# Kernel tuning notes

Hardware: AMD Instinct MI355X
Metric: run time of the kernel (lower is better)

Reference implementation:

```python
import jax, jax.numpy as jnp
import numpy as np

N_NODES, N_EDGES, D_IN, D_OUT = 50000, 800000, 64, 64
N_REL, N_TIME = 500, 1000


def setup_inputs() -> dict:
    key = jax.random.key(0)
    ks = jax.random.split(key, 14)
    xavier = lambda k, shape: jax.random.normal(k, shape, jnp.float32) * np.sqrt(2.0 / (shape[0] + shape[1])) * np.sqrt(2.0)
    return {
        "x": jax.random.normal(ks[0], (N_NODES, D_IN), jnp.float32),
        "rel_repr": jax.random.normal(ks[1], (N_REL, D_IN), jnp.float32),
        "time_emds": jax.random.normal(ks[2], (N_TIME, D_IN), jnp.float32),
        "src": jax.random.randint(ks[3], (N_EDGES,), 0, N_NODES),
        "dst": jax.random.randint(ks[4], (N_EDGES,), 0, N_NODES),
        "etype": jax.random.randint(ks[5], (N_EDGES,), 0, N_REL),
        "etime": jax.random.randint(ks[6], (N_EDGES,), 0, N_TIME),
        "trans_w": xavier(ks[7], (D_IN, D_OUT)),
        "loop_w": xavier(ks[8], (D_IN, D_OUT)),
        "w_rel": xavier(ks[9], (D_IN, D_OUT)),
        "attn_h": xavier(ks[10], (D_IN, 1)),
        "attn_t": xavier(ks[11], (D_IN, 1)),
        "attn_r": xavier(ks[12], (D_IN, 1)),
        "attn_ts": xavier(ks[13], (D_IN, 1)),
    }


def reference(x, rel_repr, time_emds, src, dst, etype, etime,
              trans_w, loop_w, w_rel, attn_h, attn_t, attn_r, attn_ts):
    n = x.shape[0]
    # per-node / per-rel / per-time scalar attention projections
    h_att = (x @ attn_h)[:, 0]          # [N]
    t_att = (x @ attn_t)[:, 0]          # [N]
    r_att = (rel_repr @ attn_r)[:, 0]   # [R]
    ts_att = (time_emds @ attn_ts)[:, 0]  # [T]
    # edge attention logits + edge_softmax grouped by destination node
    e = jax.nn.leaky_relu(h_att[src] - t_att[dst] + r_att[etype] + ts_att[etime], 0.1)  # [E]
    m = jax.ops.segment_max(e, dst, num_segments=n)
    ex = jnp.exp(e - m[dst])
    den = jax.ops.segment_sum(ex, dst, num_segments=n)
    att = (ex / den[dst])[:, None]      # [E,1]
    # message: (head + time) * (rel + time) -> trans_w -> weighted scatter-sum to dst
    time_emd = time_emds[etime]         # [E,D]
    edge_data = (x[src] + time_emd) * (rel_repr[etype] + time_emd)
    msg = (edge_data @ trans_w) * att   # [E,D_out]
    h = jax.ops.segment_sum(msg, dst, num_segments=n)
    x_out = h + x @ loop_w
    rel_out = rel_repr @ w_rel
    return (x_out, rel_out)
```

## Files before the change

### kernel.cpp

```cpp
#include <hip/hip_runtime.h>
#include <hip/hip_bf16.h>

#define N_NODES 50000
#define N_EDGES 800000
#define D 64
#define N_REL 500
#define N_TIME 1000
#define SLOTS 64
#define NODE_BLOCKS ((N_NODES + 63) / 64)
#define REL_BLOCKS  ((N_REL + 63) / 64)

__device__ __forceinline__ float bf2f(unsigned short u) {
    union { unsigned int i; float f; } v;
    v.i = ((unsigned int)u) << 16;
    return v.f;
}

__global__ void proj_kernel(const float* __restrict__ x,
                            const float* __restrict__ rel,
                            const float* __restrict__ tim,
                            const float* __restrict__ ah,
                            const float* __restrict__ at,
                            const float* __restrict__ ar,
                            const float* __restrict__ ats,
                            float* __restrict__ h_att, float* __restrict__ t_att,
                            float* __restrict__ r_att, float* __restrict__ ts_att,
                            unsigned short* __restrict__ x_bf) {
    int wave = (blockIdx.x * blockDim.x + threadIdx.x) >> 6;
    int lane = threadIdx.x & 63;
    const int total = N_NODES + N_REL + N_TIME;
    if (wave >= total) return;
    if (wave < N_NODES) {
        float xv = x[wave * D + lane];
        __hip_bfloat16 b = __float2bfloat16(xv);
        x_bf[wave * D + lane] = *(unsigned short*)&b;
        float s1 = xv * ah[lane];
        float s2 = xv * at[lane];
        for (int off = 32; off; off >>= 1) {
            s1 += __shfl_down(s1, off);
            s2 += __shfl_down(s2, off);
        }
        if (lane == 0) { h_att[wave] = s1; t_att[wave] = s2; }
    } else if (wave < N_NODES + N_REL) {
        int r = wave - N_NODES;
        float v = rel[r * D + lane] * ar[lane];
        for (int off = 32; off; off >>= 1) v += __shfl_down(v, off);
        if (lane == 0) r_att[r] = v;
    } else {
        int t = wave - N_NODES - N_REL;
        float v = tim[t * D + lane] * ats[lane];
        for (int off = 32; off; off >>= 1) v += __shfl_down(v, off);
        if (lane == 0) ts_att[t] = v;
    }
}

__global__ void build_kernel(const int* __restrict__ src, const int* __restrict__ dst,
                             const int* __restrict__ etype, const int* __restrict__ etime,
                             const float* __restrict__ h_att, const float* __restrict__ t_att,
                             const float* __restrict__ r_att, const float* __restrict__ ts_att,
                             int* __restrict__ cnt, int2* __restrict__ payload) {
    int e = blockIdx.x * blockDim.x + threadIdx.x;
    if (e >= N_EDGES) return;
    int s = src[e], d = dst[e], r = etype[e], t = etime[e];
    float lg = h_att[s] - t_att[d] + r_att[r] + ts_att[t];
    float lr = lg > 0.f ? lg : 0.1f * lg;
    float ex = __expf(lr);
    unsigned exb = __float_as_uint(ex);
    int2 pl;
    pl.x = (int)((exb & ~7u) | (unsigned)(s & 7));
    pl.y = (int)(((unsigned)(s >> 3) << 19) | ((unsigned)r << 10) | (unsigned)t);
    int pos = atomicAdd(&cnt[d], 1);
    if (pos < SLOTS) payload[(d << 6) + pos] = pl;
}

__global__ void node_gather_kernel(const unsigned short* __restrict__ x_bf,
                                   const float* __restrict__ rel,
                                   const float* __restrict__ tim,
                                   const int* __restrict__ cnt,
                                   const int2* __restrict__ payload,
                                   float* __restrict__ agg) {
    int d = (blockIdx.x * blockDim.x + threadIdx.x) >> 6;
    int lane = threadIdx.x & 63;
    if (d >= N_NODES) return;
    int deg = cnt[d];
    if (deg > SLOTS) deg = SLOTS;

    int s_l = 0, r_l = 0, t_l = 0;
    float ex = 0.f;
    if (lane < deg) {
        int2 pl = payload[(d << 6) + lane];
        unsigned px = (unsigned)pl.x;
        unsigned py = (unsigned)pl.y;
        ex = __uint_as_float(px & ~7u);
        s_l = (int)(((py >> 19) << 3) | (px & 7u));
        r_l = (int)((py >> 10) & 511u);
        t_l = (int)(py & 1023u);
    }
    float den = ex;
    for (int off = 32; off; off >>= 1) den += __shfl_xor(den, off);
    float att_l = (lane < deg) ? ex / den : 0.f;

    int qw = lane >> 4;
    int ql = lane & 15;
    float4 acc = make_float4(0.f, 0.f, 0.f, 0.f);
    for (int i = 0; i < deg; i += 4) {
        int ei = i + qw;
        int s = __shfl(s_l, ei);
        int r = __shfl(r_l, ei);
        int t = __shfl(t_l, ei);
        float att = __shfl(att_l, ei);
        float4  te = *(const float4*)(tim + t * D + ql * 4);
        ushort4 xb = *(const ushort4*)(x_bf + s * D + ql * 4);
        float4  rl = *(const float4*)(rel + r * D + ql * 4);
        acc.x += att * (bf2f(xb.x) + te.x) * (rl.x + te.x);
        acc.y += att * (bf2f(xb.y) + te.y) * (rl.y + te.y);
        acc.z += att * (bf2f(xb.z) + te.z) * (rl.z + te.z);
        acc.w += att * (bf2f(xb.w) + te.w) * (rl.w + te.w);
    }
    for (int off = 16; off <= 32; off <<= 1) {
        acc.x += __shfl_xor(acc.x, off);
        acc.y += __shfl_xor(acc.y, off);
        acc.z += __shfl_xor(acc.z, off);
        acc.w += __shfl_xor(acc.w, off);
    }
    if (qw == 0)
        *(float4*)(agg + (d << 7) + ql * 4) = acc;
}

__global__ __launch_bounds__(256, 4)
void out_gemm_kernel(const float* __restrict__ agg,
                     const float* __restrict__ x,
                     const float* __restrict__ rel,
                     const float* __restrict__ trans_w,
                     const float* __restrict__ loop_w,
                     const float* __restrict__ w_rel,
                     float* __restrict__ out) {
    __shared__ float Wa[D * D];
    __shared__ float Wb[D * D];
    int t = threadIdx.x;
    bool nodeb = blockIdx.x < NODE_BLOCKS;

    for (int j = 0; j < 4; j++) {
        int idx = (t + 256 * j) * 4;
        if (nodeb) {
            *(float4*)(Wa + idx) = *(const float4*)(trans_w + idx);
            *(float4*)(Wb + idx) = *(const float4*)(loop_w + idx);
        } else {
            *(float4*)(Wa + idx) = *(const float4*)(w_rel + idx);
        }
    }
    __syncthreads();

    int lane = t & 63;
    int wv = t >> 6;
    int c4 = (lane & 15) << 2;
    int r0 = wv * 16 + (lane >> 4) * 4;

    float acc[4][4];
    for (int i = 0; i < 4; i++)
        for (int c = 0; c < 4; c++) acc[i][c] = 0.f;

    if (nodeb) {
        int row0 = blockIdx.x * 64;
        for (int k = 0; k < D; k += 4) {
            float wt[4][4], wl[4][4];
            for (int kk = 0; kk < 4; kk++) {
                *(float4*)&wt[kk][0] = *(const float4*)(Wa + (k + kk) * D + c4);
                *(float4*)&wl[kk][0] = *(const float4*)(Wb + (k + kk) * D + c4);
            }
            for (int i = 0; i < 4; i++) {
                int gr = row0 + r0 + i;
                if (gr >= N_NODES) gr = N_NODES - 1;
                float a[4], xv[4];
                *(float4*)&a[0]  = *(const float4*)(agg + (size_t)gr * 128 + k);
                *(float4*)&xv[0] = *(const float4*)(x   + (size_t)gr * D + k);
                for (int c = 0; c < 4; c++) {
                    float s = acc[i][c];
                    for (int kk = 0; kk < 4; kk++)
                        s += a[kk] * wt[kk][c] + xv[kk] * wl[kk][c];
                    acc[i][c] = s;
                }
            }
        }
        for (int i = 0; i < 4; i++) {
            int gr = row0 + r0 + i;
            if (gr < N_NODES)
                *(float4*)(out + (size_t)gr * D + c4) = *(float4*)&acc[i][0];
        }
    } else {
        int row0 = (blockIdx.x - NODE_BLOCKS) * 64;
        for (int k = 0; k < D; k += 4) {
            float wt[4][4];
            for (int kk = 0; kk < 4; kk++)
                *(float4*)&wt[kk][0] = *(const float4*)(Wa + (k + kk) * D + c4);
            for (int i = 0; i < 4; i++) {
                int gr = row0 + r0 + i;
                if (gr >= N_REL) gr = N_REL - 1;
                float a[4];
                *(float4*)&a[0] = *(const float4*)(rel + (size_t)gr * D + k);
                for (int c = 0; c < 4; c++) {
                    float s = acc[i][c];
                    for (int kk = 0; kk < 4; kk++)
                        s += a[kk] * wt[kk][c];
                    acc[i][c] = s;
                }
            }
        }
        for (int i = 0; i < 4; i++) {
            int gr = row0 + r0 + i;
            if (gr < N_REL)
                *(float4*)(out + (size_t)(N_NODES + gr) * D + c4) = *(float4*)&acc[i][0];
        }
    }
}

extern "C" void kernel_launch(void* const* d_in, const int* in_sizes, int n_in,
                              void* d_out, int out_size, void* d_ws, size_t ws_size,
                              hipStream_t stream) {
    const float* x    = (const float*)d_in[0];
    const float* rel  = (const float*)d_in[1];
    const float* tim  = (const float*)d_in[2];
    const int* src   = (const int*)d_in[3];
    const int* dst   = (const int*)d_in[4];
    const int* etype = (const int*)d_in[5];
    const int* etime = (const int*)d_in[6];
    const float* trans_w = (const float*)d_in[7];
    const float* loop_w  = (const float*)d_in[8];
    const float* w_rel   = (const float*)d_in[9];
    const float* ah  = (const float*)d_in[10];
    const float* at  = (const float*)d_in[11];
    const float* ar  = (const float*)d_in[12];
    const float* ats = (const float*)d_in[13];

    char* ws = (char*)d_ws;
    int*   cnt            = (int*)  (ws);
    float* h_att          = (float*)(ws + 200000);
    float* t_att          = (float*)(ws + 400000);
    float* r_att          = (float*)(ws + 600000);
    float* ts_att         = (float*)(ws + 602000);
    int2*  payload        = (int2*) (ws + 1000000);
    float* agg            = (float*)(ws + 1000000);
    unsigned short* x_bf  = (unsigned short*)(ws + 26600000);

    float* out = (float*)d_out;

    hipMemsetAsync(cnt, 0, N_NODES * sizeof(int), stream);

    {
        int waves = N_NODES + N_REL + N_TIME;
        proj_kernel<<<(waves + 3) / 4, 256, 0, stream>>>(
            x, rel, tim, ah, at, ar, ats,
            h_att, t_att, r_att, ts_att, x_bf);
    }
    {
        build_kernel<<<(N_EDGES + 255) / 256, 256, 0, stream>>>(
            src, dst, etype, etime, h_att, t_att, r_att, ts_att, cnt, payload);
    }
    {
        node_gather_kernel<<<(N_NODES + 3) / 4, 256, 0, stream>>>(
            x_bf, rel, tim, cnt, payload, agg);
    }
    {
        out_gemm_kernel<<<NODE_BLOCKS + REL_BLOCKS, 256, 0, stream>>>(
            agg, x, rel, trans_w, loop_w, w_rel, out);
    }
}
```

Baseline: 207.4 us.

## Bin edges by destination range before scattering into per-node payload slots

Replaces the single edge-build pass with two phases. First, each block computes edge logits and exps, bins records into 8 destination-range buckets in shared memory, and flushes them to a staging buffer. Second, a scatter pass walks each bucket and does the per-node atomic slot insertion. The aim is to make the random atomics and payload writes hit a smaller node range at a time, which should improve cache locality. The cost is an extra kernel launch, an extra round trip of 16-byte records through global memory, and a path that depends on workspace size (it falls back to the old kernel if the workspace is too small).

```diff
diff --git a/kernel.cpp b/kernel.cpp
--- a/kernel.cpp
+++ b/kernel.cpp
@@ -9,6 +9,13 @@
 #define SLOTS 64
 #define NODE_BLOCKS ((N_NODES + 63) / 64)
 #define REL_BLOCKS  ((N_REL + 63) / 64)
+
+#define NBUCKET 8
+#define NODES_PER_BUCKET 6250
+#define STAGE_CAP 131072
+#define BIN_CAP 256
+#define TILE 1024
+#define PASS2_CHUNKS 128
 
 __device__ __forceinline__ float bf2f(unsigned short u) {
     union { unsigned int i; float f; } v;
@@ -73,6 +80,80 @@
     if (pos < SLOTS) payload[(d << 6) + pos] = pl;
 }
 
+__global__ __launch_bounds__(256)
+void bin_kernel(const int* __restrict__ src, const int* __restrict__ dst,
+                const int* __restrict__ etype, const int* __restrict__ etime,
+                const float* __restrict__ h_att, const float* __restrict__ t_att,
+                const float* __restrict__ r_att, const float* __restrict__ ts_att,
+                int* __restrict__ bucket_cursor, int4* __restrict__ stage) {
+    __shared__ int4 bins[NBUCKET][BIN_CAP];
+    __shared__ int bcnt[NBUCKET];
+    __shared__ int bbase[NBUCKET];
+    int t = threadIdx.x;
+    if (t < NBUCKET) bcnt[t] = 0;
+    __syncthreads();
+
+    int e0 = blockIdx.x * TILE;
+    for (int j = 0; j < 4; j++) {
+        int e = e0 + j * 256 + t;
+        if (e < N_EDGES) {
+            int s = src[e], d = dst[e], r = etype[e], tt = etime[e];
+            float lg = h_att[s] - t_att[d] + r_att[r] + ts_att[tt];
+            float lr = lg > 0.f ? lg : 0.1f * lg;
+            float ex = __expf(lr);
+            unsigned exb = __float_as_uint(ex);
+            int4 rec;
+            rec.x = (int)((exb & ~7u) | (unsigned)(s & 7));
+            rec.y = (int)(((unsigned)(s >> 3) << 19) | ((unsigned)r << 10) | (unsigned)tt);
+            rec.z = d;
+            rec.w = 0;
+            int k = (int)((unsigned)d / NODES_PER_BUCKET);
+            int pos = atomicAdd(&bcnt[k], 1);
+            if (pos < BIN_CAP) {
+                bins[k][pos] = rec;
+            } else {
+                int g = atomicAdd(&bucket_cursor[k], 1);
+                if (g < STAGE_CAP) stage[k * STAGE_CAP + g] = rec;
+            }
+        }
+    }
+    __syncthreads();
+    if (t < NBUCKET) {
+        int c = bcnt[t] < BIN_CAP ? bcnt[t] : BIN_CAP;
+        bbase[t] = atomicAdd(&bucket_cursor[t], c);
+        bcnt[t] = c;
+    }
+    __syncthreads();
+    for (int k = 0; k < NBUCKET; k++) {
+        int c = bcnt[k];
+        int base = bbase[k];
+        for (int idx = t; idx < c; idx += 256) {
+            int g = base + idx;
+            if (g < STAGE_CAP) stage[k * STAGE_CAP + g] = bins[k][idx];
+        }
+    }
+}
+
+__global__ __launch_bounds__(256)
+void scatter_kernel(const int* __restrict__ bucket_cursor,
+                    const int4* __restrict__ stage,
+                    int* __restrict__ cnt, int2* __restrict__ payload) {
+    int b = blockIdx.x & (NBUCKET - 1);
+    int chunk = blockIdx.x >> 3;
+    int n = bucket_cursor[b];
+    if (n > STAGE_CAP) n = STAGE_CAP;
+    int ch = (n + PASS2_CHUNKS - 1) / PASS2_CHUNKS;
+    int start = chunk * ch;
+    int end = start + ch;
+    if (end > n) end = n;
+    for (int idx = start + (int)threadIdx.x; idx < end; idx += 256) {
+        int4 rec = stage[b * STAGE_CAP + idx];
+        int d = rec.z;
+        int pos = atomicAdd(&cnt[d], 1);
+        if (pos < SLOTS) payload[(d << 6) + pos] = make_int2(rec.x, rec.y);
+    }
+}
+
 __global__ void node_gather_kernel(const unsigned short* __restrict__ x_bf,
                                    const float* __restrict__ rel,
                                    const float* __restrict__ tim,
@@ -234,17 +315,22 @@
 
     char* ws = (char*)d_ws;
     int*   cnt            = (int*)  (ws);
-    float* h_att          = (float*)(ws + 200000);
-    float* t_att          = (float*)(ws + 400000);
-    float* r_att          = (float*)(ws + 600000);
-    float* ts_att         = (float*)(ws + 602000);
+    int*   bucket_cursor  = (int*)  (ws + 200000);
+    float* h_att          = (float*)(ws + 200064);
+    float* t_att          = (float*)(ws + 400064);
+    float* r_att          = (float*)(ws + 600064);
+    float* ts_att         = (float*)(ws + 602064);
     int2*  payload        = (int2*) (ws + 1000000);
     float* agg            = (float*)(ws + 1000000);
     unsigned short* x_bf  = (unsigned short*)(ws + 26600000);
+    int4*  stage          = (int4*) (ws + 33000000);
 
     float* out = (float*)d_out;
 
-    hipMemsetAsync(cnt, 0, N_NODES * sizeof(int), stream);
+    const size_t need = 33000000ull + (size_t)NBUCKET * STAGE_CAP * sizeof(int4);
+    const bool two_phase = (ws_size >= need);
+
+    hipMemsetAsync(cnt, 0, 200032, stream);
 
     {
         int waves = N_NODES + N_REL + N_TIME;
@@ -252,7 +338,13 @@
             x, rel, tim, ah, at, ar, ats,
             h_att, t_att, r_att, ts_att, x_bf);
     }
-    {
+    if (two_phase) {
+        bin_kernel<<<(N_EDGES + TILE - 1) / TILE, 256, 0, stream>>>(
+            src, dst, etype, etime, h_att, t_att, r_att, ts_att,
+            bucket_cursor, stage);
+        scatter_kernel<<<NBUCKET * PASS2_CHUNKS, 256, 0, stream>>>(
+            bucket_cursor, stage, cnt, payload);
+    } else {
         build_kernel<<<(N_EDGES + 255) / 256, 256, 0, stream>>>(
             src, dst, etype, etime, h_att, t_att, r_att, ts_att, cnt, payload);
     }
```

After: 219.3 us. 1.06x slower.
